# Performance work log

Hardware: AMD Instinct MI355X
Metric: run time of the kernel (lower is better)

Reference implementation:

```python
import jax, jax.numpy as jnp
import numpy as np

H = 4  # hidden size fixed by the module


def setup_inputs() -> dict:
    key = jax.random.key(0)
    ks = jax.random.split(key, 7)
    B, T, I = 4096, 1024, 8
    s_ih = 1.0 / np.sqrt(H)
    return {
        "x": jax.random.normal(ks[0], (B, T, I), dtype=jnp.float32),
        "W_ih": jax.random.uniform(ks[1], (4 * H, I), jnp.float32, -s_ih, s_ih),
        "W_hh": jax.random.uniform(ks[2], (4 * H, H), jnp.float32, -s_ih, s_ih),
        "b_ih": jax.random.uniform(ks[3], (4 * H,), jnp.float32, -s_ih, s_ih),
        "b_hh": jax.random.uniform(ks[4], (4 * H,), jnp.float32, -s_ih, s_ih),
        "fc_w": jax.random.uniform(ks[5], (1, H), jnp.float32, -0.5, 0.5),
        "fc_b": jax.random.uniform(ks[6], (1,), jnp.float32, -0.5, 0.5),
    }


def _lstm_last_hidden(x, W_ih, W_hh, b_ih, b_hh):
    B = x.shape[0]
    # Precompute input contribution for all timesteps: [B, T, 4H] -> scan over T
    xg = jnp.einsum("bti,gi->btg", x, W_ih) + (b_ih + b_hh)
    xg = jnp.swapaxes(xg, 0, 1)  # [T, B, 4H]

    def step(carry, g_t):
        h, c = carry
        gates = g_t + h @ W_hh.T  # [B, 4H]
        i, f, g, o = jnp.split(gates, 4, axis=-1)  # PyTorch gate order
        c = jax.nn.sigmoid(f) * c + jax.nn.sigmoid(i) * jnp.tanh(g)
        h = jax.nn.sigmoid(o) * jnp.tanh(c)
        return (h, c), None

    h0 = jnp.zeros((B, H), dtype=x.dtype)
    (h_last, _), _ = jax.lax.scan(step, (h0, h0), xg)
    return h_last  # [B, H]


def reference(x, W_ih, W_hh, b_ih, b_hh, fc_w, fc_b):
    h_last = _lstm_last_hidden(x, W_ih, W_hh, b_ih, b_hh)
    return h_last @ fc_w.T + fc_b  # [B, 1]
```

## Files before the change

kernel.cpp:

```cpp
#include <hip/hip_runtime.h>


#define TT 1024
#define II 8
#define CHUNK 32
#define NCHUNK (TT / CHUNK)
#define ROW (CHUNK * II)
#define SPAD 4

#define L2E 1.4426950408889634f
#define SIG_SCALE (-L2E)
#define G_SCALE (2.0f * L2E)

typedef float v2f __attribute__((ext_vector_type(2)));

template <int CTRL>
__device__ __forceinline__ float dppf(float v) {
  return __int_as_float(
      __builtin_amdgcn_mov_dpp(__float_as_int(v), CTRL, 0xF, 0xF, true));
}

__device__ __forceinline__ float ex2(float x) {
  return __builtin_amdgcn_exp2f(x);
}
__device__ __forceinline__ float rcp(float x) {
  return __builtin_amdgcn_rcpf(x);
}

#define GLOAD_LDS16(gp, lp)                                   \
  __builtin_amdgcn_global_load_lds(                           \
      (const __attribute__((address_space(1))) void*)(gp),    \
      (__attribute__((address_space(3))) void*)(lp), 16, 0, 0)

__global__ __launch_bounds__(128, 1) void lstm_fused(
    const float* __restrict__ x, const float* __restrict__ W_ih,
    const float* __restrict__ W_hh, const float* __restrict__ b_ih,
    const float* __restrict__ b_hh, const float* __restrict__ fc_w,
    const float* __restrict__ fc_b, float* __restrict__ out, int B) {
  const int tid = threadIdx.x;
  const int wave = tid >> 6;
  const int lane = tid & 63;
  const int j = lane & 3;
  const int grp = lane >> 2;
  const int b = blockIdx.x * 16 + grp;

  __shared__ float xs0[16][ROW + SPAD];
  __shared__ float xs1[16][ROW + SPAD];
  __shared__ float pa0[CHUNK][16][16];
  __shared__ float pa1[CHUNK][16][16];

  if (wave == 0) {
    v2f wih01[II], wih23[II];
    v2f bias01, bias23;
#pragma unroll
    for (int k = 0; k < II; ++k) {
      wih01[k] = v2f{SIG_SCALE * W_ih[(0 * 4 + j) * II + k],
                     SIG_SCALE * W_ih[(1 * 4 + j) * II + k]};
      wih23[k] = v2f{G_SCALE * W_ih[(2 * 4 + j) * II + k],
                     SIG_SCALE * W_ih[(3 * 4 + j) * II + k]};
    }
    bias01 = v2f{SIG_SCALE * (b_ih[0 * 4 + j] + b_hh[0 * 4 + j]),
                 SIG_SCALE * (b_ih[1 * 4 + j] + b_hh[1 * 4 + j])};
    bias23 = v2f{G_SCALE * (b_ih[2 * 4 + j] + b_hh[2 * 4 + j]),
                 SIG_SCALE * (b_ih[3 * 4 + j] + b_hh[3 * 4 + j])};

    const size_t blockBase = (size_t)blockIdx.x * 16;

    auto issue = [&](float(*xs)[ROW + SPAD], int t0) {
#pragma unroll
      for (int s = 0; s < 16; ++s) {
        const float* gp =
            x + (blockBase + s) * (TT * II) + (size_t)t0 * II + lane * 4;
        GLOAD_LDS16(gp, &xs[s][0]);
      }
    };

    auto produce = [&](float(*pa)[16][16], const float(*xs)[ROW + SPAD]) {
      const float* row = &xs[grp][0];
#pragma unroll 8
      for (int u = 0; u < CHUNK; ++u) {
        const float4 xa = *(const float4*)(row + u * 8);
        const float4 xb = *(const float4*)(row + u * 8 + 4);
        v2f a01 = bias01, a23 = bias23;
#define XFMA(k, val)                                    \
  {                                                     \
    v2f xv = v2f{(val), (val)};                         \
    a01 = __builtin_elementwise_fma(wih01[k], xv, a01); \
    a23 = __builtin_elementwise_fma(wih23[k], xv, a23); \
  }
        XFMA(0, xa.x) XFMA(1, xa.y) XFMA(2, xa.z) XFMA(3, xa.w)
        XFMA(4, xb.x) XFMA(5, xb.y) XFMA(6, xb.z) XFMA(7, xb.w)
#undef XFMA
        *(float4*)&pa[u][grp][j * 4] = float4{a01.x, a01.y, a23.x, a23.y};
      }
    };

    issue(xs0, 0);
    issue(xs1, CHUNK);
    produce(pa0, xs0);
    __syncthreads();

    for (int ck = 0; ck < NCHUNK; ++ck) {
      if (ck + 1 < NCHUNK)
        produce(((ck + 1) & 1) ? pa1 : pa0, ((ck + 1) & 1) ? xs1 : xs0);
      if (ck + 2 < NCHUNK) issue((ck & 1) ? xs1 : xs0, (ck + 2) * CHUNK);
      __syncthreads();
    }
  } else {
    v2f whh01[4], whh23[4];
#pragma unroll
    for (int k = 0; k < 4; ++k) {
      whh01[k] = v2f{SIG_SCALE * W_hh[(0 * 4 + j) * 4 + k],
                     SIG_SCALE * W_hh[(1 * 4 + j) * 4 + k]};
      whh23[k] = v2f{G_SCALE * W_hh[(2 * 4 + j) * 4 + k],
                     SIG_SCALE * W_hh[(3 * 4 + j) * 4 + k]};
    }
    float h = 0.0f, c2 = 0.0f;

    auto step = [&](float4 g) {
      const float h0 = dppf<0x00>(h);
      const float h1 = dppf<0x55>(h);
      const float h2 = dppf<0xAA>(h);
      const float h3 = dppf<0xFF>(h);
      v2f a01 = v2f{g.x, g.y};
      v2f a23 = v2f{g.z, g.w};
#define HFMA(k, val)                                    \
  {                                                     \
    v2f hv = v2f{(val), (val)};                         \
    a01 = __builtin_elementwise_fma(whh01[k], hv, a01); \
    a23 = __builtin_elementwise_fma(whh23[k], hv, a23); \
  }
      HFMA(0, h0) HFMA(1, h1) HFMA(2, h2) HFMA(3, h3)
#undef HFMA
      const float ig = rcp(1.0f + ex2(a01.x));
      const float fg = rcp(1.0f + ex2(a01.y));
      const float rg = rcp(1.0f + ex2(a23.x));
      const float og = rcp(1.0f + ex2(a23.y));
      const float gg2 = fmaf(rg, -2.0f * G_SCALE, G_SCALE);
      c2 = fmaf(fg, c2, ig * gg2);
      const float rc = rcp(1.0f + ex2(c2));
      const float m2og = -2.0f * og;
      h = fmaf(rc, m2og, og);
    };

    __syncthreads();

    for (int ck = 0; ck < NCHUNK; ++ck) {
      const float(*pa)[16][16] = (ck & 1) ? pa1 : pa0;
      const float* base = &pa[0][grp][j * 4];

      float4 ra[8], rb[8];
#define LOADB(r, u0)                                                \
  {                                                                 \
    _Pragma("unroll") for (int k = 0; k < 8; ++k) (r)[k] =          \
        *(const float4*)(base + (u0 + k) * 256);                    \
  }
#define COMP8(r)                                   \
  { _Pragma("unroll") for (int k = 0; k < 8; ++k) step((r)[k]); }

      LOADB(ra, 0)
      LOADB(rb, 8)
      COMP8(ra)
      LOADB(ra, 16)
      COMP8(rb)
      LOADB(rb, 24)
      COMP8(ra)
      COMP8(rb)
#undef LOADB
#undef COMP8
      __syncthreads();
    }

    float v = h * fc_w[j];
    v += dppf<0xB1>(v);
    v += dppf<0x4E>(v);
    if (j == 0 && b < B) out[b] = v + fc_b[0];
  }
}

extern "C" void kernel_launch(void* const* d_in, const int* in_sizes, int n_in,
                              void* d_out, int out_size, void* d_ws,
                              size_t ws_size, hipStream_t stream) {
  const float* x = (const float*)d_in[0];
  const float* W_ih = (const float*)d_in[1];
  const float* W_hh = (const float*)d_in[2];
  const float* b_ih = (const float*)d_in[3];
  const float* b_hh = (const float*)d_in[4];
  const float* fc_w = (const float*)d_in[5];
  const float* fc_b = (const float*)d_in[6];
  float* out = (float*)d_out;

  const int B = in_sizes[0] / (TT * II);
  const int nblocks = (B + 15) / 16;
  lstm_fused<<<nblocks, 128, 0, stream>>>(x, W_ih, W_hh, b_ih, b_hh, fc_w,
                                          fc_b, out, B);
}
```

Measured before the change: 259.8 us.

## Pack four producer/consumer wave pairs per block with finer-grained chunks

```diff
diff --git a/kernel.cpp b/kernel.cpp
--- a/kernel.cpp
+++ b/kernel.cpp
@@ -3,9 +3,10 @@
 
 #define TT 1024
 #define II 8
-#define CHUNK 32
-#define NCHUNK (TT / CHUNK)
-#define ROW (CHUNK * II)
+#define SCH 32
+#define PCH 8
+#define NROUND (TT / PCH)
+#define ROW (SCH * II)
 #define SPAD 4
 
 #define L2E 1.4426950408889634f
@@ -32,24 +33,24 @@
       (const __attribute__((address_space(1))) void*)(gp),    \
       (__attribute__((address_space(3))) void*)(lp), 16, 0, 0)
 
-__global__ __launch_bounds__(128, 1) void lstm_fused(
+__global__ __launch_bounds__(512, 1) void lstm_fused(
     const float* __restrict__ x, const float* __restrict__ W_ih,
     const float* __restrict__ W_hh, const float* __restrict__ b_ih,
     const float* __restrict__ b_hh, const float* __restrict__ fc_w,
     const float* __restrict__ fc_b, float* __restrict__ out, int B) {
   const int tid = threadIdx.x;
-  const int wave = tid >> 6;
+  const int wv = tid >> 6;
+  const int role = wv >> 2;
+  const int p = wv & 3;
   const int lane = tid & 63;
   const int j = lane & 3;
   const int grp = lane >> 2;
-  const int b = blockIdx.x * 16 + grp;
+  const int b = blockIdx.x * 64 + p * 16 + grp;
 
-  __shared__ float xs0[16][ROW + SPAD];
-  __shared__ float xs1[16][ROW + SPAD];
-  __shared__ float pa0[CHUNK][16][16];
-  __shared__ float pa1[CHUNK][16][16];
+  __shared__ float xs[4][16][ROW + SPAD];
+  __shared__ float pa[4][2][PCH][16][16];
 
-  if (wave == 0) {
+  if (role == 0) {
     v2f wih01[II], wih23[II];
     v2f bias01, bias23;
 #pragma unroll
@@ -64,21 +65,22 @@
     bias23 = v2f{G_SCALE * (b_ih[2 * 4 + j] + b_hh[2 * 4 + j]),
                  SIG_SCALE * (b_ih[3 * 4 + j] + b_hh[3 * 4 + j])};
 
-    const size_t blockBase = (size_t)blockIdx.x * 16;
+    const size_t sbase = (size_t)blockIdx.x * 64 + (size_t)p * 16;
 
-    auto issue = [&](float(*xs)[ROW + SPAD], int t0) {
+    auto issue = [&](int t0) {
 #pragma unroll
       for (int s = 0; s < 16; ++s) {
-        const float* gp =
-            x + (blockBase + s) * (TT * II) + (size_t)t0 * II + lane * 4;
-        GLOAD_LDS16(gp, &xs[s][0]);
+        size_t si = sbase + s;
+        si = (si < (size_t)B) ? si : (size_t)(B - 1);
+        const float* gp = x + si * (TT * II) + (size_t)t0 * II + lane * 4;
+        GLOAD_LDS16(gp, &xs[p][s][0]);
       }
     };
 
-    auto produce = [&](float(*pa)[16][16], const float(*xs)[ROW + SPAD]) {
-      const float* row = &xs[grp][0];
-#pragma unroll 8
-      for (int u = 0; u < CHUNK; ++u) {
+    auto produce = [&](float(*pab)[16][16], int off) {
+      const float* row = &xs[p][grp][off];
+#pragma unroll
+      for (int u = 0; u < PCH; ++u) {
         const float4 xa = *(const float4*)(row + u * 8);
         const float4 xb = *(const float4*)(row + u * 8 + 4);
         v2f a01 = bias01, a23 = bias23;
@@ -91,19 +93,20 @@
         XFMA(0, xa.x) XFMA(1, xa.y) XFMA(2, xa.z) XFMA(3, xa.w)
         XFMA(4, xb.x) XFMA(5, xb.y) XFMA(6, xb.z) XFMA(7, xb.w)
 #undef XFMA
-        *(float4*)&pa[u][grp][j * 4] = float4{a01.x, a01.y, a23.x, a23.y};
+        *(float4*)&pab[u][grp][j * 4] = float4{a01.x, a01.y, a23.x, a23.y};
       }
     };
 
-    issue(xs0, 0);
-    issue(xs1, CHUNK);
-    produce(pa0, xs0);
+    issue(0);
+    produce(pa[p][0], 0);
     __syncthreads();
 
-    for (int ck = 0; ck < NCHUNK; ++ck) {
-      if (ck + 1 < NCHUNK)
-        produce(((ck + 1) & 1) ? pa1 : pa0, ((ck + 1) & 1) ? xs1 : xs0);
-      if (ck + 2 < NCHUNK) issue((ck & 1) ? xs1 : xs0, (ck + 2) * CHUNK);
+    for (int m = 0; m < NROUND; ++m) {
+      const int c = m + 1;
+      if (c < NROUND) {
+        produce(pa[p][c & 1], (c & 3) * (PCH * II));
+        if ((c & 3) == 3 && c + 1 < NROUND) issue((c + 1) * PCH);
+      }
       __syncthreads();
     }
   } else {
@@ -139,35 +142,22 @@
       const float gg2 = fmaf(rg, -2.0f * G_SCALE, G_SCALE);
       c2 = fmaf(fg, c2, ig * gg2);
       const float rc = rcp(1.0f + ex2(c2));
-      const float m2og = -2.0f * og;
-      h = fmaf(rc, m2og, og);
+      h = fmaf(rc, -2.0f * og, og);
     };
 
     __syncthreads();
 
-    for (int ck = 0; ck < NCHUNK; ++ck) {
-      const float(*pa)[16][16] = (ck & 1) ? pa1 : pa0;
-      const float* base = &pa[0][grp][j * 4];
-
-      float4 ra[8], rb[8];
-#define LOADB(r, u0)                                                \
-  {                                                                 \
-    _Pragma("unroll") for (int k = 0; k < 8; ++k) (r)[k] =          \
-        *(const float4*)(base + (u0 + k) * 256);                    \
-  }
-#define COMP8(r)                                   \
-  { _Pragma("unroll") for (int k = 0; k < 8; ++k) step((r)[k]); }
-
-      LOADB(ra, 0)
-      LOADB(rb, 8)
-      COMP8(ra)
-      LOADB(ra, 16)
-      COMP8(rb)
-      LOADB(rb, 24)
-      COMP8(ra)
-      COMP8(rb)
-#undef LOADB
-#undef COMP8
+    for (int m = 0; m < NROUND; ++m) {
+      const float(*pab)[16][16] = pa[p][m & 1];
+      const float* base = &pab[0][grp][j * 4];
+      float4 g = *(const float4*)base;
+#pragma unroll
+      for (int u = 0; u < PCH; ++u) {
+        const int un = (u + 1 < PCH) ? (u + 1) : u;
+        const float4 gn = *(const float4*)(base + un * 256);
+        step(g);
+        g = gn;
+      }
       __syncthreads();
     }
 
@@ -191,7 +181,7 @@
   float* out = (float*)d_out;
 
   const int B = in_sizes[0] / (TT * II);
-  const int nblocks = (B + 15) / 16;
-  lstm_fused<<<nblocks, 128, 0, stream>>>(x, W_ih, W_hh, b_ih, b_hh, fc_w,
+  const int nblocks = (B + 63) / 64;
+  lstm_fused<<<nblocks, 512, 0, stream>>>(x, W_ih, W_hh, b_ih, b_hh, fc_w,
                                           fc_b, out, B);
 }
```

New measurement: 322.6 us. 1.24x slower.
